# Kernel tuning notes

Measured on AMD Instinct MI355X. Metric: run time of the kernel, lower is better.

## Reference

```python
import jax, jax.numpy as jnp
import numpy as np

KERNEL = 25  # hard-coded moving-average kernel in the torch Model
HID = 128


def moving_avg(x):
    # x: [B, L, C]; edge-pad (KERNEL-1)//2 on each side along time, then mean over window
    p = (KERNEL - 1) // 2
    front = jnp.repeat(x[:, 0:1, :], p, axis=1)
    end = jnp.repeat(x[:, -1:, :], p, axis=1)
    xp = jnp.concatenate([front, x, end], axis=1)  # [B, L+2p, C]
    cs = jnp.cumsum(xp, axis=1)
    cs = jnp.concatenate([jnp.zeros_like(cs[:, :1, :]), cs], axis=1)
    return (cs[:, KERNEL:, :] - cs[:, :-KERNEL, :]) / KERNEL  # [B, L, C]


def memory_enhance(repres, memory):
    # repres: [N, 128], memory: [F, 128]
    attention = jax.nn.softmax(jnp.einsum('nd,fd->nf', repres, memory), axis=1)
    output = jnp.einsum('nf,fd->nd', attention, memory)
    return jnp.concatenate([output, repres], axis=1)  # [N, 256]


def setup_inputs() -> dict:
    key = jax.random.key(0)
    ks = jax.random.split(key, 12)
    B, L, C, P, M = 128, 720, 321, 336, 512
    s = lambda k, shape, fan: jax.random.normal(k, shape, jnp.float32) * (1.0 / np.sqrt(fan))
    return {
        'x': jax.random.normal(ks[0], (B, L, C), jnp.float32),
        'W_s1': s(ks[1], (HID, L), L), 'b_s1': jnp.zeros((HID,), jnp.float32),
        'W_s2': s(ks[2], (P, 2 * HID), 2 * HID), 'b_s2': jnp.zeros((P,), jnp.float32),
        'W_t1': s(ks[3], (HID, L), L), 'b_t1': jnp.zeros((HID,), jnp.float32),
        'W_t2': s(ks[4], (P, 2 * HID), 2 * HID), 'b_t2': jnp.zeros((P,), jnp.float32),
        'mem_S': s(ks[5], (M, HID), HID),
        'mem_T': s(ks[6], (M, HID), HID),
    }


def reference(x, W_s1, b_s1, W_s2, b_s2, W_t1, b_t1, W_t2, b_t2, mem_S, mem_T):
    B, L, C = x.shape
    trend = moving_avg(x)                 # [B, L, C]
    seasonal = x - trend
    seasonal = jnp.transpose(seasonal, (0, 2, 1))  # [B, C, L]
    trend = jnp.transpose(trend, (0, 2, 1))

    def branch(init, W1, b1, mem, W2, b2):
        r = jax.nn.sigmoid(jnp.einsum('bcl,hl->bch', init, W1) + b1)  # [B, C, 128]
        r = r.reshape(-1, HID)
        r = memory_enhance(r, mem)                                    # [N, 256]
        r = r.reshape(B, C, 2 * HID)
        return jnp.einsum('bcd,pd->bcp', r, W2) + b2                  # [B, C, P]

    seasonal_out = branch(seasonal, W_s1, b_s1, mem_S, W_s2, b_s2)
    trend_out = branch(trend, W_t1, b_t1, mem_T, W_t2, b_t2)
    return jnp.transpose(seasonal_out + trend_out, (0, 2, 1))  # [B, P, C]
```

## Files before the change

### kernel.cpp

```cpp
#include <hip/hip_runtime.h>
#include <math.h>

#define BB 128
#define LL 720
#define CC 321
#define HH 128
#define PP 336
#define MM 512
#define NSTEP 23

typedef __attribute__((ext_vector_type(8))) short bf16x8;
typedef __attribute__((ext_vector_type(4))) float f32x4;

__device__ __forceinline__ short f2bf(float x) {
  unsigned u = __builtin_bit_cast(unsigned, x);
  u = (u + 0x7FFFu + ((u >> 16) & 1u)) >> 16;
  return (short)u;
}

__device__ __forceinline__ int packpos(int kw) {
  return ((kw & 15) >> 2) * 8 + (kw >> 4) * 4 + (kw & 3);
}

__device__ __forceinline__ void gload_lds16(const short* g, short* l) {
  __builtin_amdgcn_global_load_lds(
      (const __attribute__((address_space(1))) unsigned int*)g,
      (__attribute__((address_space(3))) unsigned int*)l, 16, 0, 0);
}

__global__ void weff_kernel(const float* __restrict__ Ws1,
                            const float* __restrict__ Wt1,
                            short* __restrict__ wimg) {
  int idx = blockIdx.x * 256 + threadIdx.x;
  if (idx >= HH * NSTEP * 32) return;
  int j = idx % (NSTEP * 32), h = idx / (NSTEP * 32);
  int s = j >> 5, kw = j & 31;
  int half = kw >> 4, lg = (kw >> 2) & 3, jj = kw & 3;
  size_t base = ((size_t)(s * 128 + h)) * 64 + half * 4 + jj;
  int slotS = (0 + lg) ^ (h & 7);
  int slotT = (4 + lg) ^ (h & 7);
  if (j >= LL) {
    wimg[base + slotS * 8] = 0;
    wimg[base + slotT * 8] = 0;
    return;
  }
  float ss = 0.f, st = 0.f;
  if (j == 0) {
    for (int l = 0; l <= 12; ++l) {
      float w = 13.f - (float)l;
      ss += w * Ws1[h * LL + l];
      st += w * Wt1[h * LL + l];
    }
  } else if (j == LL - 1) {
    for (int d = 0; d <= 12; ++d) {
      float w = 13.f - (float)d;
      ss += w * Ws1[h * LL + LL - 1 - d];
      st += w * Wt1[h * LL + LL - 1 - d];
    }
  } else {
    int lo = j - 12 < 0 ? 0 : j - 12;
    int hi = j + 12 > LL - 1 ? LL - 1 : j + 12;
    for (int l = lo; l <= hi; ++l) {
      ss += Ws1[h * LL + l];
      st += Wt1[h * LL + l];
    }
  }
  ss *= (1.f / 25.f);
  st *= (1.f / 25.f);
  wimg[base + slotS * 8] = f2bf(Ws1[h * LL + j] - ss);
  wimg[base + slotT * 8] = f2bf(st);
}

__global__ void memstage_kernel(const float* __restrict__ memS,
                                const float* __restrict__ memT,
                                short* __restrict__ stgS,
                                short* __restrict__ stgT) {
  int e = blockIdx.x * 256 + threadIdx.x;
  int br = e >> 14;
  int s = e & 16383;
  const float* src = br ? memT : memS;
  short* dst = br ? stgT : stgS;
  int tt = s >> 11;
  int c = s & 2047;
  int row = c >> 4, slot = c & 15;
  int sp = slot ^ (row & 7);
  int k = sp >> 2, lg = sp & 3;
  int ft = tt >> 1;
  short out[8];
  if ((tt & 1) == 0) {
    const float* r0 = src + (size_t)(ft * 128 + row) * 128 + k * 32 + lg * 4;
#pragma unroll
    for (int j = 0; j < 4; ++j) {
      out[j] = f2bf(r0[j]);
      out[j + 4] = f2bf(r0[16 + j]);
    }
  } else {
    int fbase = ft * 128 + k * 32 + lg * 4;
#pragma unroll
    for (int j = 0; j < 4; ++j) {
      out[j] = f2bf(src[(size_t)(fbase + j) * 128 + row]);
      out[j + 4] = f2bf(src[(size_t)(fbase + 16 + j) * 128 + row]);
    }
  }
  short4 a = make_short4(out[0], out[1], out[2], out[3]);
  short4 b = make_short4(out[4], out[5], out[6], out[7]);
  *(short4*)&dst[(size_t)s * 8] = a;
  *(short4*)&dst[(size_t)s * 8 + 4] = b;
}

__global__ void w2cvt_kernel(const float* __restrict__ Ws2,
                             const float* __restrict__ Wt2,
                             const float* __restrict__ bs2,
                             const float* __restrict__ bt2,
                             short* __restrict__ W2b, float* __restrict__ b2) {
  int i = blockIdx.x * 256 + threadIdx.x;
  if (i < PP) b2[i] = bs2[i] + bt2[i];
  if (i >= PP * 512) return;
  int p = i >> 9, k = i & 511;
  float v = (k < 256) ? Ws2[p * 256 + k] : Wt2[p * 256 + (k - 256)];
  W2b[p * 512 + (k >> 5) * 32 + packpos(k & 31)] = f2bf(v);
}

__global__ __launch_bounds__(256, 4) void gemm1_mfma(
    const float* __restrict__ x, const short* __restrict__ wimg,
    const float* __restrict__ bs1, const float* __restrict__ bt1,
    short* __restrict__ r2s, short* __restrict__ r2t) {
  __shared__ __align__(16) short wbuf[2][8192];
  __shared__ __align__(16) short xbuf[2][1024];
  int tid = threadIdx.x;
  int w = tid >> 6, l = tid & 63, lr = l & 15, lg = l >> 4;
  int br = w >> 1, hb = (w & 1) * 64;
  int nb = blockIdx.x * 32;

  int xcol = tid & 31, krow = tid >> 5;
  int xn = nb + xcol;
  int xb_ = xn / CC, xc_ = xn - xb_ * CC;
  const float* xptr = x + (size_t)xb_ * (LL * CC) + xc_;
  int xrow = xcol >> 1;
  int xslot = ((xcol & 1) * 4 + (krow & 3)) ^ (xrow & 7);
  int xdst = xrow * 64 + xslot * 8 + (krow >> 2) * 4;

  const short* wsrc = wimg + (size_t)w * 2048 + l * 8;

  f32x4 acc[4][2];
#pragma unroll
  for (int i = 0; i < 4; ++i)
#pragma unroll
    for (int g = 0; g < 2; ++g) acc[i][g] = (f32x4){0.f, 0.f, 0.f, 0.f};

  {
#pragma unroll
    for (int i = 0; i < 4; ++i)
      gload_lds16(wsrc + i * 512, &wbuf[0][w * 2048 + i * 512]);
    float xf[4];
#pragma unroll
    for (int j = 0; j < 4; ++j) xf[j] = xptr[(size_t)(krow * 4 + j) * CC];
    short4 v = make_short4(f2bf(xf[0]), f2bf(xf[1]), f2bf(xf[2]), f2bf(xf[3]));
    *(short4*)&xbuf[0][xdst] = v;
  }
  __syncthreads();

  int cur = 0;
  for (int s = 0; s < NSTEP; ++s) {
    float xf[4];
    if (s < NSTEP - 1) {
      int kbase = (s + 1) * 32 + krow * 4;
#pragma unroll
      for (int j = 0; j < 4; ++j) {
        int k = kbase + j;
        xf[j] = (k < LL) ? xptr[(size_t)k * CC] : 0.f;
      }
      const short* ws = wsrc + (size_t)(s + 1) * 8192;
#pragma unroll
      for (int i = 0; i < 4; ++i)
        gload_lds16(ws + i * 512, &wbuf[cur ^ 1][w * 2048 + i * 512]);
    }

    const short* tw = &wbuf[cur][0];
    const short* tx = &xbuf[cur][0];
    bf16x8 bx[2];
#pragma unroll
    for (int g = 0; g < 2; ++g) {
      int cc = g * 16 + lr;
      int row = cc >> 1;
      int slot = ((cc & 1) * 4 + lg) ^ (row & 7);
      bx[g] = *(const bf16x8*)&tx[row * 64 + slot * 8];
    }
#pragma unroll
    for (int ht = 0; ht < 4; ++ht) {
      int h = hb + ht * 16 + lr;
      int slot = (br * 4 + lg) ^ (h & 7);
      bf16x8 a = *(const bf16x8*)&tw[h * 64 + slot * 8];
      acc[ht][0] =
          __builtin_amdgcn_mfma_f32_16x16x32_bf16(a, bx[0], acc[ht][0], 0, 0, 0);
      acc[ht][1] =
          __builtin_amdgcn_mfma_f32_16x16x32_bf16(a, bx[1], acc[ht][1], 0, 0, 0);
    }

    if (s < NSTEP - 1) {
      short4 v = make_short4(f2bf(xf[0]), f2bf(xf[1]), f2bf(xf[2]), f2bf(xf[3]));
      *(short4*)&xbuf[cur ^ 1][xdst] = v;
    }
    __syncthreads();
    cur ^= 1;
  }

  const float* bias = br ? bt1 : bs1;
  short* r2 = br ? r2t : r2s;
#pragma unroll
  for (int ht = 0; ht < 4; ++ht) {
    int h0 = hb + ht * 16 + lg * 4;
    int dst = (h0 >> 5) * 32 + lg * 8 + ((h0 >> 4) & 1) * 4;
    float4 bi = *(const float4*)&bias[h0];
    const float* pb = &bi.x;
#pragma unroll
    for (int g = 0; g < 2; ++g) {
      int n = nb + g * 16 + lr;
      short4 v;
      short* pv = &v.x;
#pragma unroll
      for (int j = 0; j < 4; ++j)
        pv[j] = f2bf(1.f / (1.f + __expf(-(acc[ht][g][j] + pb[j]))));
      *(short4*)&r2[(size_t)n * 256 + 128 + dst] = v;
    }
  }
}

__global__ __launch_bounds__(256) void memenh_mfma(
    const short* __restrict__ stgS, const short* __restrict__ stgT,
    short* __restrict__ r2s, short* __restrict__ r2t) {
  int br = blockIdx.y;
  const short* stg = br ? stgT : stgS;
  short* r2 = br ? r2t : r2s;

  __shared__ __align__(16) short buf[2][16384];
  int tid = threadIdx.x;
  int l = tid & 63, lr = l & 15, lg = l >> 4;
  int wbase = tid & 192;
  int n = blockIdx.x * 64 + (tid >> 6) * 16 + lr;

  bf16x8 brag[4];
  {
    const short* rb = r2 + (size_t)n * 256 + 128;
#pragma unroll
    for (int k = 0; k < 4; ++k)
      brag[k] = *(const bf16x8*)&rb[k * 32 + lg * 8];
  }

#define STAGE(t, bsel)                                                        \
  {                                                                           \
    const short* g = stg + (size_t)(t)*16384;                                 \
    _Pragma("unroll") for (int i = 0; i < 8; ++i) {                           \
      gload_lds16(g + (size_t)(i * 256 + tid) * 8,                            \
                  &buf[bsel][(i * 256 + wbase) * 8]);                         \
    }                                                                         \
  }

  STAGE(0, 0);
  __syncthreads();

  f32x4 accO[8];
#pragma unroll
  for (int i = 0; i < 8; ++i) accO[i] = (f32x4){0.f, 0.f, 0.f, 0.f};
  bf16x8 pb[4];
  float ssum = 0.f;
  int cur = 0;

#pragma unroll
  for (int t = 0; t < 8; ++t) {
    if (t < 7) STAGE(t + 1, cur ^ 1);
    const short* tb = &buf[cur][0];
    if ((t & 1) == 0) {
      f32x4 sc[8];
#pragma unroll
      for (int ft16 = 0; ft16 < 8; ++ft16) {
        f32x4 a = {0.f, 0.f, 0.f, 0.f};
#pragma unroll
        for (int k = 0; k < 4; ++k) {
          int row = ft16 * 16 + lr;
          int slot = (4 * k + lg) ^ (row & 7);
          bf16x8 af = *(const bf16x8*)&tb[row * 128 + slot * 8];
          a = __builtin_amdgcn_mfma_f32_16x16x32_bf16(af, brag[k], a, 0, 0, 0);
        }
        sc[ft16] = a;
      }
#pragma unroll
      for (int i = 0; i < 8; ++i) {
        f32x4 v = sc[i];
#pragma unroll
        for (int j = 0; j < 4; ++j) {
          float e = __expf(v[j]);
          v[j] = e;
          ssum += e;
        }
        sc[i] = v;
      }
#pragma unroll
      for (int t4 = 0; t4 < 4; ++t4) {
        f32x4 e0 = sc[2 * t4], e1 = sc[2 * t4 + 1];
        bf16x8 f;
        f[0] = f2bf(e0[0]); f[1] = f2bf(e0[1]);
        f[2] = f2bf(e0[2]); f[3] = f2bf(e0[3]);
        f[4] = f2bf(e1[0]); f[5] = f2bf(e1[1]);
        f[6] = f2bf(e1[2]); f[7] = f2bf(e1[3]);
        pb[t4] = f;
      }
    } else {
#pragma unroll
      for (int dt = 0; dt < 8; ++dt) {
#pragma unroll
        for (int k = 0; k < 4; ++k) {
          int row = dt * 16 + lr;
          int slot = (4 * k + lg) ^ (row & 7);
          bf16x8 af = *(const bf16x8*)&tb[row * 128 + slot * 8];
          accO[dt] =
              __builtin_amdgcn_mfma_f32_16x16x32_bf16(af, pb[k], accO[dt], 0, 0, 0);
        }
      }
    }
    __syncthreads();
    cur ^= 1;
  }
#undef STAGE

  ssum += __shfl_xor(ssum, 16);
  ssum += __shfl_xor(ssum, 32);
  float inv = 1.f / ssum;
  short* rowO = r2 + (size_t)n * 256;
#pragma unroll
  for (int dt = 0; dt < 8; ++dt) {
    short4 o;
    o.x = f2bf(accO[dt][0] * inv);
    o.y = f2bf(accO[dt][1] * inv);
    o.z = f2bf(accO[dt][2] * inv);
    o.w = f2bf(accO[dt][3] * inv);
    *(short4*)&rowO[(dt >> 1) * 32 + lg * 8 + (dt & 1) * 4] = o;
  }
}

__global__ __launch_bounds__(512) void gemm2_mfma(
    const short* __restrict__ r2s, const short* __restrict__ r2t,
    const short* __restrict__ W2b,
    const float* __restrict__ b2,
    float* __restrict__ out) {
  __shared__ __align__(16) short w2lds[2][112 * 40];
  int tid = threadIdx.x;
  int w = tid >> 6, l = tid & 63, lr = l & 15, lg = l >> 4;
  int p0 = blockIdx.y * 112;
  int n = blockIdx.x * 128 + w * 16 + lr;
  int b = n / CC, c = n - b * CC;
  const short* rs = r2s + (size_t)n * 256;
  const short* rt = r2t + (size_t)n * 256;

  bool dostage = tid < 448;
  int row = tid >> 2, q = tid & 3;
  const short* gW = W2b + (size_t)(p0 + row) * 512 + q * 8;
  int doff = row * 40 + q * 8;

  f32x4 acc[7];
#pragma unroll
  for (int i = 0; i < 7; ++i) acc[i] = (f32x4){0.f, 0.f, 0.f, 0.f};

  if (dostage) *(int4*)&w2lds[0][doff] = *(const int4*)gW;
  __syncthreads();

  int cur = 0;
  for (int step = 0; step < 16; ++step) {
    int k0 = step * 32;
    const short* rrow = ((k0 < 256) ? rs : rt) + (k0 & 255);
    bf16x8 bfr = *(const bf16x8*)&rrow[lg * 8];
    int4 nxt = {0, 0, 0, 0};
    if (step < 15 && dostage) nxt = *(const int4*)(gW + (step + 1) * 32);
    const short* tw = &w2lds[cur][0];
#pragma unroll
    for (int pt = 0; pt < 7; ++pt) {
      bf16x8 a = *(const bf16x8*)&tw[(pt * 16 + lr) * 40 + lg * 8];
      acc[pt] = __builtin_amdgcn_mfma_f32_16x16x32_bf16(a, bfr, acc[pt], 0, 0, 0);
    }
    if (step < 15 && dostage) *(int4*)&w2lds[cur ^ 1][doff] = nxt;
    __syncthreads();
    cur ^= 1;
  }

  size_t obase = (size_t)b * ((size_t)PP * CC) + c;
#pragma unroll
  for (int pt = 0; pt < 7; ++pt) {
    int p = p0 + pt * 16 + lg * 4;
    float4 bias = *(const float4*)&b2[p];
    const float* pb = &bias.x;
#pragma unroll
    for (int j = 0; j < 4; ++j) {
      out[obase + (size_t)(p + j) * CC] = acc[pt][j] + pb[j];
    }
  }
}

extern "C" void kernel_launch(void* const* d_in, const int* in_sizes, int n_in,
                              void* d_out, int out_size, void* d_ws, size_t ws_size,
                              hipStream_t stream) {
  const float* x    = (const float*)d_in[0];
  const float* Ws1  = (const float*)d_in[1];
  const float* bs1  = (const float*)d_in[2];
  const float* Ws2  = (const float*)d_in[3];
  const float* bs2  = (const float*)d_in[4];
  const float* Wt1  = (const float*)d_in[5];
  const float* bt1  = (const float*)d_in[6];
  const float* Wt2  = (const float*)d_in[7];
  const float* bt2  = (const float*)d_in[8];
  const float* memS = (const float*)d_in[9];
  const float* memT = (const float*)d_in[10];
  float* out = (float*)d_out;

  const size_t N = (size_t)BB * CC;
  short* r2s  = (short*)d_ws;
  short* r2t  = r2s + N * 256;
  short* wimg = r2t + N * 256;
  short* stgS = wimg + (size_t)NSTEP * 128 * 64;
  short* stgT = stgS + (size_t)16384 * 8;
  short* W2b  = stgT + (size_t)16384 * 8;
  float* b2   = (float*)(W2b + (size_t)PP * 512);

  weff_kernel<<<(HH * NSTEP * 32 + 255) / 256, 256, 0, stream>>>(Ws1, Wt1, wimg);
  memstage_kernel<<<128, 256, 0, stream>>>(memS, memT, stgS, stgT);
  w2cvt_kernel<<<(PP * 512) / 256, 256, 0, stream>>>(Ws2, Wt2, bs2, bt2, W2b, b2);

  gemm1_mfma<<<1284, 256, 0, stream>>>(x, wimg, bs1, bt1, r2s, r2t);

  dim3 g3(642, 2);
  memenh_mfma<<<g3, 256, 0, stream>>>(stgS, stgT, r2s, r2t);

  dim3 g2(321, 3);
  gemm2_mfma<<<g2, 512, 0, stream>>>(r2s, r2t, W2b, b2, out);
}
```

Measured before the change: 141.6 us.

## Triple-buffer gemm1 loads with two-step prefetch and manual vmcnt waits

Converts the gemm1 main loop from double to triple buffering. Weight and x tiles are now prefetched two K-steps ahead, and __syncthreads is replaced by explicit s_waitcnt vmcnt(8)/lgkmcnt(0) plus a raw barrier, so outstanding global loads can stay in flight across the barrier. The aim is to hide global-memory latency better. In exchange it uses more LDS and drops the 4-blocks-per-CU launch bound, which may lower occupancy. The hand-counted vmcnt values are also fragile if the compiler emits a different number of loads.

```diff
diff --git a/kernel.cpp b/kernel.cpp
--- a/kernel.cpp
+++ b/kernel.cpp
@@ -27,6 +27,17 @@
       (const __attribute__((address_space(1))) unsigned int*)g,
       (__attribute__((address_space(3))) unsigned int*)l, 16, 0, 0);
 }
+
+#define VMCNT8 asm volatile("s_waitcnt vmcnt(8)" ::: "memory")
+#define VMCNT0 asm volatile("s_waitcnt vmcnt(0)" ::: "memory")
+#define LGKM0 asm volatile("s_waitcnt lgkmcnt(0)" ::: "memory")
+#define RAWBAR                                \
+  do {                                        \
+    __builtin_amdgcn_sched_barrier(0);        \
+    __builtin_amdgcn_s_barrier();             \
+    __builtin_amdgcn_sched_barrier(0);        \
+    asm volatile("" ::: "memory");            \
+  } while (0)
 
 __global__ void weff_kernel(const float* __restrict__ Ws1,
                             const float* __restrict__ Wt1,
@@ -121,12 +132,12 @@
   W2b[p * 512 + (k >> 5) * 32 + packpos(k & 31)] = f2bf(v);
 }
 
-__global__ __launch_bounds__(256, 4) void gemm1_mfma(
+__global__ __launch_bounds__(256) void gemm1_mfma(
     const float* __restrict__ x, const short* __restrict__ wimg,
     const float* __restrict__ bs1, const float* __restrict__ bt1,
     short* __restrict__ r2s, short* __restrict__ r2t) {
-  __shared__ __align__(16) short wbuf[2][8192];
-  __shared__ __align__(16) short xbuf[2][1024];
+  __shared__ __align__(16) short wbuf[3][8192];
+  __shared__ __align__(16) short xbuf[3][1024];
   int tid = threadIdx.x;
   int w = tid >> 6, l = tid & 63, lr = l & 15, lg = l >> 4;
   int br = w >> 1, hb = (w & 1) * 64;
@@ -148,61 +159,84 @@
 #pragma unroll
     for (int g = 0; g < 2; ++g) acc[i][g] = (f32x4){0.f, 0.f, 0.f, 0.f};
 
+  float xf0[4], xfA[4], xfB[4];
+
+#pragma unroll
+  for (int j = 0; j < 4; ++j) xf0[j] = xptr[(size_t)(krow * 4 + j) * CC];
+#pragma unroll
+  for (int i = 0; i < 4; ++i)
+    gload_lds16(wsrc + i * 512, &wbuf[0][w * 2048 + i * 512]);
+#pragma unroll
+  for (int j = 0; j < 4; ++j)
+    xfA[j] = xptr[(size_t)(32 + krow * 4 + j) * CC];
+#pragma unroll
+  for (int i = 0; i < 4; ++i)
+    gload_lds16(wsrc + 8192 + i * 512, &wbuf[1][w * 2048 + i * 512]);
   {
-#pragma unroll
-    for (int i = 0; i < 4; ++i)
-      gload_lds16(wsrc + i * 512, &wbuf[0][w * 2048 + i * 512]);
-    float xf[4];
-#pragma unroll
-    for (int j = 0; j < 4; ++j) xf[j] = xptr[(size_t)(krow * 4 + j) * CC];
-    short4 v = make_short4(f2bf(xf[0]), f2bf(xf[1]), f2bf(xf[2]), f2bf(xf[3]));
+    short4 v = make_short4(f2bf(xf0[0]), f2bf(xf0[1]), f2bf(xf0[2]),
+                           f2bf(xf0[3]));
     *(short4*)&xbuf[0][xdst] = v;
   }
-  __syncthreads();
-
-  int cur = 0;
+  VMCNT8;
+  LGKM0;
+  RAWBAR;
+
+  int bc = 0, bn = 1, bi = 2;
   for (int s = 0; s < NSTEP; ++s) {
-    float xf[4];
+    if (s < NSTEP - 2) {
+      int kb = (s + 2) * 32 + krow * 4;
+#pragma unroll
+      for (int j = 0; j < 4; ++j) {
+        int k = kb + j;
+        xfB[j] = (k < LL) ? xptr[(size_t)k * CC] : 0.f;
+      }
+      const short* ws = wsrc + (size_t)(s + 2) * 8192;
+#pragma unroll
+      for (int i = 0; i < 4; ++i)
+        gload_lds16(ws + i * 512, &wbuf[bi][w * 2048 + i * 512]);
+    }
+
+    {
+      const short* tw = &wbuf[bc][0];
+      const short* tx = &xbuf[bc][0];
+      bf16x8 bx[2];
+#pragma unroll
+      for (int g = 0; g < 2; ++g) {
+        int cc = g * 16 + lr;
+        int row = cc >> 1;
+        int slot = ((cc & 1) * 4 + lg) ^ (row & 7);
+        bx[g] = *(const bf16x8*)&tx[row * 64 + slot * 8];
+      }
+#pragma unroll
+      for (int ht = 0; ht < 4; ++ht) {
+        int h = hb + ht * 16 + lr;
+        int slot = (br * 4 + lg) ^ (h & 7);
+        bf16x8 a = *(const bf16x8*)&tw[h * 64 + slot * 8];
+        acc[ht][0] = __builtin_amdgcn_mfma_f32_16x16x32_bf16(a, bx[0],
+                                                             acc[ht][0], 0, 0, 0);
+        acc[ht][1] = __builtin_amdgcn_mfma_f32_16x16x32_bf16(a, bx[1],
+                                                             acc[ht][1], 0, 0, 0);
+      }
+    }
+
     if (s < NSTEP - 1) {
-      int kbase = (s + 1) * 32 + krow * 4;
-#pragma unroll
-      for (int j = 0; j < 4; ++j) {
-        int k = kbase + j;
-        xf[j] = (k < LL) ? xptr[(size_t)k * CC] : 0.f;
-      }
-      const short* ws = wsrc + (size_t)(s + 1) * 8192;
-#pragma unroll
-      for (int i = 0; i < 4; ++i)
-        gload_lds16(ws + i * 512, &wbuf[cur ^ 1][w * 2048 + i * 512]);
-    }
-
-    const short* tw = &wbuf[cur][0];
-    const short* tx = &xbuf[cur][0];
-    bf16x8 bx[2];
-#pragma unroll
-    for (int g = 0; g < 2; ++g) {
-      int cc = g * 16 + lr;
-      int row = cc >> 1;
-      int slot = ((cc & 1) * 4 + lg) ^ (row & 7);
-      bx[g] = *(const bf16x8*)&tx[row * 64 + slot * 8];
-    }
-#pragma unroll
-    for (int ht = 0; ht < 4; ++ht) {
-      int h = hb + ht * 16 + lr;
-      int slot = (br * 4 + lg) ^ (h & 7);
-      bf16x8 a = *(const bf16x8*)&tw[h * 64 + slot * 8];
-      acc[ht][0] =
-          __builtin_amdgcn_mfma_f32_16x16x32_bf16(a, bx[0], acc[ht][0], 0, 0, 0);
-      acc[ht][1] =
-          __builtin_amdgcn_mfma_f32_16x16x32_bf16(a, bx[1], acc[ht][1], 0, 0, 0);
-    }
-
-    if (s < NSTEP - 1) {
-      short4 v = make_short4(f2bf(xf[0]), f2bf(xf[1]), f2bf(xf[2]), f2bf(xf[3]));
-      *(short4*)&xbuf[cur ^ 1][xdst] = v;
-    }
-    __syncthreads();
-    cur ^= 1;
+      short4 v = make_short4(f2bf(xfA[0]), f2bf(xfA[1]), f2bf(xfA[2]),
+                             f2bf(xfA[3]));
+      *(short4*)&xbuf[bn][xdst] = v;
+      if (s < NSTEP - 2) {
+        VMCNT8;
+      } else {
+        VMCNT0;
+      }
+      LGKM0;
+      RAWBAR;
+#pragma unroll
+      for (int j = 0; j < 4; ++j) xfA[j] = xfB[j];
+    }
+    int t = bc;
+    bc = bn;
+    bn = bi;
+    bi = t;
   }
 
   const float* bias = br ? bt1 : bs1;
@@ -211,8 +245,8 @@
   for (int ht = 0; ht < 4; ++ht) {
     int h0 = hb + ht * 16 + lg * 4;
     int dst = (h0 >> 5) * 32 + lg * 8 + ((h0 >> 4) & 1) * 4;
-    float4 bi = *(const float4*)&bias[h0];
-    const float* pb = &bi.x;
+    float4 bi4 = *(const float4*)&bias[h0];
+    const float* pb = &bi4.x;
 #pragma unroll
     for (int g = 0; g < 2; ++g) {
       int n = nb + g * 16 + lr;
```

After: 151.6 us. 7.0% more time.

## Pre-stage x into bf16 swizzled image and double gemm1 N-tile to 64

Applied to the files above, without the earlier changes.

A new xstage kernel converts x to bf16 and writes it in the LDS-swizzled tile layout, so gemm1 can pull x tiles with direct async global-to-LDS copies instead of strided fp32 loads and in-kernel conversion. gemm1's per-block N tile grows from 32 to 64 columns, so each weight tile is reused across twice as many columns and half as many blocks are launched. This adds an extra pass that writes and rereads a bf16 copy of x, plus more accumulator registers per thread, which may lower occupancy. The launch-bounds occupancy hint is also dropped.

```diff
diff --git a/kernel.cpp b/kernel.cpp
--- a/kernel.cpp
+++ b/kernel.cpp
@@ -69,6 +69,34 @@
   st *= (1.f / 25.f);
   wimg[base + slotS * 8] = f2bf(Ws1[h * LL + j] - ss);
   wimg[base + slotT * 8] = f2bf(st);
+}
+
+__global__ void xstage_kernel(const float* __restrict__ x,
+                              short* __restrict__ ximg) {
+  int blk = blockIdx.x, s = blockIdx.y;
+  int t = threadIdx.x;
+  int n = blk * 64 + t;
+  int b = n / CC, c = n - b * CC;
+  const float* xp = x + (size_t)b * (LL * CC) + c;
+  float v[32];
+  int k0 = s * 32;
+#pragma unroll
+  for (int kk = 0; kk < 32; ++kk) {
+    int k = k0 + kk;
+    v[kk] = (k < LL) ? xp[(size_t)k * CC] : 0.f;
+  }
+  short* dst = ximg + ((size_t)(blk * NSTEP + s)) * 2048;
+  int row = t >> 1;
+#pragma unroll
+  for (int lg = 0; lg < 4; ++lg) {
+    int slot = ((t & 1) * 4 + lg) ^ (row & 7);
+    short4 lo = make_short4(f2bf(v[lg * 4 + 0]), f2bf(v[lg * 4 + 1]),
+                            f2bf(v[lg * 4 + 2]), f2bf(v[lg * 4 + 3]));
+    short4 hi = make_short4(f2bf(v[16 + lg * 4 + 0]), f2bf(v[16 + lg * 4 + 1]),
+                            f2bf(v[16 + lg * 4 + 2]), f2bf(v[16 + lg * 4 + 3]));
+    *(short4*)&dst[(row * 8 + slot) * 8] = lo;
+    *(short4*)&dst[(row * 8 + slot) * 8 + 4] = hi;
+  }
 }
 
 __global__ void memstage_kernel(const float* __restrict__ memS,
@@ -121,89 +149,70 @@
   W2b[p * 512 + (k >> 5) * 32 + packpos(k & 31)] = f2bf(v);
 }
 
-__global__ __launch_bounds__(256, 4) void gemm1_mfma(
-    const float* __restrict__ x, const short* __restrict__ wimg,
+__global__ __launch_bounds__(256) void gemm1_mfma(
+    const short* __restrict__ wimg, const short* __restrict__ ximg,
     const float* __restrict__ bs1, const float* __restrict__ bt1,
     short* __restrict__ r2s, short* __restrict__ r2t) {
   __shared__ __align__(16) short wbuf[2][8192];
-  __shared__ __align__(16) short xbuf[2][1024];
+  __shared__ __align__(16) short xbuf[2][2048];
   int tid = threadIdx.x;
   int w = tid >> 6, l = tid & 63, lr = l & 15, lg = l >> 4;
   int br = w >> 1, hb = (w & 1) * 64;
-  int nb = blockIdx.x * 32;
-
-  int xcol = tid & 31, krow = tid >> 5;
-  int xn = nb + xcol;
-  int xb_ = xn / CC, xc_ = xn - xb_ * CC;
-  const float* xptr = x + (size_t)xb_ * (LL * CC) + xc_;
-  int xrow = xcol >> 1;
-  int xslot = ((xcol & 1) * 4 + (krow & 3)) ^ (xrow & 7);
-  int xdst = xrow * 64 + xslot * 8 + (krow >> 2) * 4;
+  int blk = blockIdx.x;
+  int nb = blk * 64;
 
   const short* wsrc = wimg + (size_t)w * 2048 + l * 8;
-
-  f32x4 acc[4][2];
+  const short* xsrc = ximg + (size_t)blk * NSTEP * 2048 + tid * 8;
+  short* xdstU = &xbuf[0][0];
+
+  f32x4 acc[4][4];
 #pragma unroll
   for (int i = 0; i < 4; ++i)
 #pragma unroll
-    for (int g = 0; g < 2; ++g) acc[i][g] = (f32x4){0.f, 0.f, 0.f, 0.f};
-
-  {
-#pragma unroll
-    for (int i = 0; i < 4; ++i)
-      gload_lds16(wsrc + i * 512, &wbuf[0][w * 2048 + i * 512]);
-    float xf[4];
-#pragma unroll
-    for (int j = 0; j < 4; ++j) xf[j] = xptr[(size_t)(krow * 4 + j) * CC];
-    short4 v = make_short4(f2bf(xf[0]), f2bf(xf[1]), f2bf(xf[2]), f2bf(xf[3]));
-    *(short4*)&xbuf[0][xdst] = v;
-  }
+    for (int g = 0; g < 4; ++g) acc[i][g] = (f32x4){0.f, 0.f, 0.f, 0.f};
+
+#define STAGE(ss, bb)                                                     \
+  do {                                                                    \
+    const short* ws_ = wsrc + (size_t)(ss)*8192;                          \
+    _Pragma("unroll") for (int i = 0; i < 4; ++i)                         \
+        gload_lds16(ws_ + i * 512, &wbuf[bb][w * 2048 + i * 512]);        \
+    gload_lds16(xsrc + (size_t)(ss)*2048, &xbuf[bb][(tid & 192) * 8]);    \
+  } while (0)
+
+  STAGE(0, 0);
   __syncthreads();
 
   int cur = 0;
   for (int s = 0; s < NSTEP; ++s) {
-    float xf[4];
-    if (s < NSTEP - 1) {
-      int kbase = (s + 1) * 32 + krow * 4;
-#pragma unroll
-      for (int j = 0; j < 4; ++j) {
-        int k = kbase + j;
-        xf[j] = (k < LL) ? xptr[(size_t)k * CC] : 0.f;
-      }
-      const short* ws = wsrc + (size_t)(s + 1) * 8192;
-#pragma unroll
-      for (int i = 0; i < 4; ++i)
-        gload_lds16(ws + i * 512, &wbuf[cur ^ 1][w * 2048 + i * 512]);
-    }
+    if (s < NSTEP - 1) STAGE(s + 1, cur ^ 1);
 
     const short* tw = &wbuf[cur][0];
     const short* tx = &xbuf[cur][0];
-    bf16x8 bx[2];
-#pragma unroll
-    for (int g = 0; g < 2; ++g) {
-      int cc = g * 16 + lr;
-      int row = cc >> 1;
-      int slot = ((cc & 1) * 4 + lg) ^ (row & 7);
-      bx[g] = *(const bf16x8*)&tx[row * 64 + slot * 8];
-    }
+    bf16x8 afr[4], bfr[4];
 #pragma unroll
     for (int ht = 0; ht < 4; ++ht) {
       int h = hb + ht * 16 + lr;
       int slot = (br * 4 + lg) ^ (h & 7);
-      bf16x8 a = *(const bf16x8*)&tw[h * 64 + slot * 8];
-      acc[ht][0] =
-          __builtin_amdgcn_mfma_f32_16x16x32_bf16(a, bx[0], acc[ht][0], 0, 0, 0);
-      acc[ht][1] =
-          __builtin_amdgcn_mfma_f32_16x16x32_bf16(a, bx[1], acc[ht][1], 0, 0, 0);
-    }
-
-    if (s < NSTEP - 1) {
-      short4 v = make_short4(f2bf(xf[0]), f2bf(xf[1]), f2bf(xf[2]), f2bf(xf[3]));
-      *(short4*)&xbuf[cur ^ 1][xdst] = v;
-    }
+      afr[ht] = *(const bf16x8*)&tw[h * 64 + slot * 8];
+    }
+#pragma unroll
+    for (int ng = 0; ng < 4; ++ng) {
+      int nl = ng * 16 + lr;
+      int row = nl >> 1;
+      int slot = ((nl & 1) * 4 + lg) ^ (row & 7);
+      bfr[ng] = *(const bf16x8*)&tx[row * 64 + slot * 8];
+    }
+#pragma unroll
+    for (int ht = 0; ht < 4; ++ht)
+#pragma unroll
+      for (int ng = 0; ng < 4; ++ng)
+        acc[ht][ng] = __builtin_amdgcn_mfma_f32_16x16x32_bf16(
+            afr[ht], bfr[ng], acc[ht][ng], 0, 0, 0);
+
     __syncthreads();
     cur ^= 1;
   }
+#undef STAGE
 
   const float* bias = br ? bt1 : bs1;
   short* r2 = br ? r2t : r2s;
@@ -211,16 +220,16 @@
   for (int ht = 0; ht < 4; ++ht) {
     int h0 = hb + ht * 16 + lg * 4;
     int dst = (h0 >> 5) * 32 + lg * 8 + ((h0 >> 4) & 1) * 4;
-    float4 bi = *(const float4*)&bias[h0];
-    const float* pb = &bi.x;
-#pragma unroll
-    for (int g = 0; g < 2; ++g) {
-      int n = nb + g * 16 + lr;
+    float4 bi4 = *(const float4*)&bias[h0];
+    const float* pb = &bi4.x;
+#pragma unroll
+    for (int ng = 0; ng < 4; ++ng) {
+      int n = nb + ng * 16 + lr;
       short4 v;
       short* pv = &v.x;
 #pragma unroll
       for (int j = 0; j < 4; ++j)
-        pv[j] = f2bf(1.f / (1.f + __expf(-(acc[ht][g][j] + pb[j]))));
+        pv[j] = f2bf(1.f / (1.f + __expf(-(acc[ht][ng][j] + pb[j]))));
       *(short4*)&r2[(size_t)n * 256 + 128 + dst] = v;
     }
   }
@@ -419,12 +428,16 @@
   short* stgT = stgS + (size_t)16384 * 8;
   short* W2b  = stgT + (size_t)16384 * 8;
   float* b2   = (float*)(W2b + (size_t)PP * 512);
+  short* ximg = (short*)(b2 + PP);
 
   weff_kernel<<<(HH * NSTEP * 32 + 255) / 256, 256, 0, stream>>>(Ws1, Wt1, wimg);
   memstage_kernel<<<128, 256, 0, stream>>>(memS, memT, stgS, stgT);
   w2cvt_kernel<<<(PP * 512) / 256, 256, 0, stream>>>(Ws2, Wt2, bs2, bt2, W2b, b2);
 
-  gemm1_mfma<<<1284, 256, 0, stream>>>(x, wimg, bs1, bt1, r2s, r2t);
+  dim3 gx(642, NSTEP);
+  xstage_kernel<<<gx, 64, 0, stream>>>(x, ximg);
+
+  gemm1_mfma<<<642, 256, 0, stream>>>(wimg, ximg, bs1, bt1, r2s, r2t);
 
   dim3 g3(642, 2);
   memenh_mfma<<<g3, 256, 0, stream>>>(stgS, stgT, r2s, r2t);
```

Result: slower. 158.6 us (+12.0%).
